# Kernel tuning notes

Measured on AMD Instinct MI355X. Metric: run time of the kernel, lower is better.

The kernel has to match this reference:

```python
import jax, jax.numpy as jnp
import numpy as np

QLEN, BSZ, DM, NH, DH, FF = 1024, 4, 512, 8, 64, 2048
EPS = 1e-5


def layer_norm(x, g, b):
    mu = x.mean(-1, keepdims=True)
    var = ((x - mu) ** 2).mean(-1, keepdims=True)
    return (x - mu) / jnp.sqrt(var + EPS) * g + b


def rel_pos_emb(qlen, klen, d_model, bsz):
    # XLNet-style 'bi' relative positional encoding: positions klen .. -qlen+1
    freq = jnp.arange(0, d_model, 2, dtype=jnp.float32)
    inv_freq = 1.0 / (10000.0 ** (freq / d_model))
    pos_seq = jnp.arange(klen, -qlen, -1, dtype=jnp.float32)  # [klen+qlen]
    sinusoid = pos_seq[:, None] * inv_freq[None, :]           # [klen+qlen, d/2]
    pe = jnp.concatenate([jnp.sin(sinusoid), jnp.cos(sinusoid)], -1)
    return jnp.broadcast_to(pe[:, None, :], (pe.shape[0], bsz, d_model))


def rel_shift(x, klen):
    # x: [q, p, b, n] with p = klen + qlen
    q, p, b, n = x.shape
    x = x.reshape(p, q, b, n)[1:]
    x = x.reshape(q, p - 1, b, n)[:, :klen]
    return x


def setup_inputs() -> dict:
    key = jax.random.key(0)
    ks = jax.random.split(key, 20)
    s = 0.02
    inp = {
        'src': jax.random.normal(ks[0], (QLEN, BSZ, DM), jnp.float32),
        'q_w': jax.random.normal(ks[1], (DM, NH, DH), jnp.float32) * s,
        'k_w': jax.random.normal(ks[2], (DM, NH, DH), jnp.float32) * s,
        'v_w': jax.random.normal(ks[3], (DM, NH, DH), jnp.float32) * s,
        'r_w': jax.random.normal(ks[4], (DM, NH, DH), jnp.float32) * s,
        'o_w': jax.random.normal(ks[5], (DM, NH, DH), jnp.float32) * s,
        'r_w_bias': jax.random.normal(ks[6], (NH, DH), jnp.float32) * s,
        'r_r_bias': jax.random.normal(ks[7], (NH, DH), jnp.float32) * s,
        'w1': jax.random.normal(ks[8], (FF, DM), jnp.float32) * s,
        'b1': jnp.zeros((FF,), jnp.float32),
        'w2': jax.random.normal(ks[9], (DM, FF), jnp.float32) * s,
        'b2': jnp.zeros((DM,), jnp.float32),
        'g1': jnp.ones((DM,), jnp.float32), 'be1': jnp.zeros((DM,), jnp.float32),
        'g2': jnp.ones((DM,), jnp.float32), 'be2': jnp.zeros((DM,), jnp.float32),
        'gf': jnp.ones((DM,), jnp.float32), 'bf': jnp.zeros((DM,), jnp.float32),
        'src_mask': jnp.triu(jnp.ones((QLEN, QLEN), bool), k=1),
    }
    return inp


def reference(src, q_w, k_w, v_w, r_w, o_w, r_w_bias, r_r_bias,
              w1, b1, w2, b2, g1, be1, g2, be2, gf, bf, src_mask):
    qlen, bsz, dm = src.shape
    klen = qlen  # mems=None
    scale = 1.0 / (DH ** 0.5)
    pos_emb = rel_pos_emb(qlen, klen, dm, bsz)  # [klen+qlen, b, d]
    mask = src_mask.astype(src.dtype)

    # --- RelativeMultiheadAttention (single weight-shared encoder layer) ---
    cat = src  # no memory
    q_head = jnp.einsum('ibh,hnd->ibnd', src, q_w)
    k_head = jnp.einsum('ibh,hnd->ibnd', cat, k_w)
    v_head = jnp.einsum('ibh,hnd->ibnd', cat, v_w)
    k_pos = jnp.einsum('ibh,hnd->ibnd', pos_emb, r_w)

    ac = jnp.einsum('ibnd,jbnd->ijbn', q_head + r_w_bias, k_head)
    bd = jnp.einsum('ibnd,jbnd->ijbn', q_head + r_r_bias, k_pos)
    bd = rel_shift(bd, klen)

    score = (ac + bd) * scale - 1e30 * mask[:, :, None, None]
    prob = jax.nn.softmax(score, axis=1)
    attn_vec = jnp.einsum('ijbn,jbnd->ibnd', prob, v_head)
    attn_out = jnp.einsum('ibnd,hnd->ibh', attn_vec, o_w)

    x = layer_norm(src + attn_out, g1, be1)
    ffn = jax.nn.gelu(x @ w1.T + b1, approximate=False) @ w2.T + b2
    x = layer_norm(x + ffn, g2, be2)

    # final encoder norm
    out = layer_norm(x, gf, bf)
    return out
```

## Files before the change

### kernel.cpp

```cpp
#include <hip/hip_runtime.h>

#define QLEN 1024
#define BSZ  4
#define DM   512
#define NH   8
#define DH   64
#define FFD  2048

static constexpr float LN_EPS = 1e-5f;

typedef __attribute__((ext_vector_type(8))) short short8_t;
typedef __attribute__((ext_vector_type(4))) float f32x4;

__device__ __forceinline__ ushort f2b(float f) {
  uint u = __float_as_uint(f);
  return (ushort)((u + 0x7FFFu + ((u >> 16) & 1u)) >> 16);
}
__device__ __forceinline__ float b2f(ushort h) {
  return __uint_as_float(((uint)h) << 16);
}

__global__ void pe_kernel(ushort* __restrict__ pe) {
  int idx = blockIdx.x * 256 + threadIdx.x;
  if (idx >= QLEN * DM) return;
  int r  = idx >> 9;
  int f  = idx & (DM - 1);
  int f0 = f & 255;
  float invf = __expf(-(float)f0 * (9.210340371976184f / 256.0f));
  float arg  = (float)r * invf;
  pe[idx] = f2b((f < 256) ? __sinf(arg) : __cosf(arg));
}

__global__ void cvt8_kernel(const float* __restrict__ in, ushort* __restrict__ out, int n8) {
  int idx = blockIdx.x * 256 + threadIdx.x;
  if (idx >= n8) return;
  const float4 f0 = *reinterpret_cast<const float4*>(in + (size_t)idx * 8);
  const float4 f1 = *reinterpret_cast<const float4*>(in + (size_t)idx * 8 + 4);
  uint p0 = f2b(f0.x) | ((uint)f2b(f0.y) << 16);
  uint p1 = f2b(f0.z) | ((uint)f2b(f0.w) << 16);
  uint p2 = f2b(f1.x) | ((uint)f2b(f1.y) << 16);
  uint p3 = f2b(f1.z) | ((uint)f2b(f1.w) << 16);
  int4 st; st.x = (int)p0; st.y = (int)p1; st.z = (int)p2; st.w = (int)p3;
  *reinterpret_cast<int4*>(out + (size_t)idx * 8) = st;
}

__global__ __launch_bounds__(256) void trans512_kernel(
    const float* __restrict__ qw, const float* __restrict__ kw,
    const float* __restrict__ vw, const float* __restrict__ rw,
    ushort* __restrict__ qkvw, ushort* __restrict__ rwT) {
  __shared__ float tile[32][33];
  const int z = blockIdx.z;
  const float* in = (z == 0) ? qw : (z == 1) ? kw : (z == 2) ? vw : rw;
  const int nd0 = blockIdx.x * 32, h0 = blockIdx.y * 32;
  const int tx = threadIdx.x & 31, ty = threadIdx.x >> 5;
#pragma unroll
  for (int k = 0; k < 4; ++k)
    tile[ty + 8 * k][tx] = in[(size_t)(h0 + ty + 8 * k) * 512 + nd0 + tx];
  __syncthreads();
  ushort* out = (z < 3) ? (qkvw + (size_t)z * 512 * 512) : rwT;
#pragma unroll
  for (int k = 0; k < 4; ++k)
    out[(size_t)(nd0 + ty + 8 * k) * 512 + h0 + tx] = f2b(tile[tx][ty + 8 * k]);
}

template <int EPI>
__global__ __launch_bounds__(256) void gemm_bf16(
    const ushort* __restrict__ A, const ushort* __restrict__ B,
    const float* __restrict__ bias, void* __restrict__ Cout,
    int M, int N, int K) {
  __shared__ ushort As[64 * 40];
  __shared__ ushort Bs[128 * 40];
  const int t = threadIdx.x;
  const int w = t >> 6, l = t & 63;
  const int lc = l & 15, lq = l >> 4;
  const int bm = blockIdx.y * 64, bn = blockIdx.x * 128;
  const int wr = (w >> 1) * 32, wc = (w & 1) * 64;
  const int sr = t >> 2, sk = (t & 3) * 8;

  f32x4 acc[2][4];
#pragma unroll
  for (int i = 0; i < 2; ++i)
#pragma unroll
    for (int j = 0; j < 4; ++j) acc[i][j] = (f32x4){0.f, 0.f, 0.f, 0.f};

  int4 a_v = *reinterpret_cast<const int4*>(A + (size_t)(bm + sr) * K + sk);
  int4 b0v = *reinterpret_cast<const int4*>(B + (size_t)(bn + sr) * K + sk);
  int4 b1v = *reinterpret_cast<const int4*>(B + (size_t)(bn + 64 + sr) * K + sk);

  for (int k0 = 0; k0 < K; k0 += 32) {
    *reinterpret_cast<int4*>(As + sr * 40 + sk) = a_v;
    *reinterpret_cast<int4*>(Bs + sr * 40 + sk) = b0v;
    *reinterpret_cast<int4*>(Bs + (64 + sr) * 40 + sk) = b1v;
    __syncthreads();
    if (k0 + 32 < K) {
      a_v = *reinterpret_cast<const int4*>(A + (size_t)(bm + sr) * K + k0 + 32 + sk);
      b0v = *reinterpret_cast<const int4*>(B + (size_t)(bn + sr) * K + k0 + 32 + sk);
      b1v = *reinterpret_cast<const int4*>(B + (size_t)(bn + 64 + sr) * K + k0 + 32 + sk);
    }
    short8_t af[2], bf[4];
#pragma unroll
    for (int mf = 0; mf < 2; ++mf)
      af[mf] = *reinterpret_cast<const short8_t*>(As + (wr + mf * 16 + lc) * 40 + lq * 8);
#pragma unroll
    for (int nf = 0; nf < 4; ++nf)
      bf[nf] = *reinterpret_cast<const short8_t*>(Bs + (wc + nf * 16 + lc) * 40 + lq * 8);
#pragma unroll
    for (int mf = 0; mf < 2; ++mf)
#pragma unroll
      for (int nf = 0; nf < 4; ++nf)
        acc[mf][nf] = __builtin_amdgcn_mfma_f32_16x16x32_bf16(af[mf], bf[nf], acc[mf][nf], 0, 0, 0);
    __syncthreads();
  }

#pragma unroll
  for (int mf = 0; mf < 2; ++mf)
#pragma unroll
    for (int nf = 0; nf < 4; ++nf) {
      const int col = bn + wc + nf * 16 + lc;
#pragma unroll
      for (int reg = 0; reg < 4; ++reg) {
        const int row = bm + wr + mf * 16 + lq * 4 + reg;
        float v = acc[mf][nf][reg];
        if (EPI == 2 || EPI == 3) v += bias[col];
        if (EPI == 2) v = 0.5f * v * (1.0f + erff(v * 0.70710678118654752f));
        if (EPI == 0 || EPI == 2)
          ((ushort*)Cout)[(size_t)row * N + col] = f2b(v);
        else
          ((float*)Cout)[(size_t)row * N + col] = v;
      }
    }
}

template <int EPI>
__global__ __launch_bounds__(256) void gemm128(
    const ushort* __restrict__ A, const ushort* __restrict__ B,
    const float* __restrict__ bias, void* __restrict__ Cout,
    int M, int N, int K) {
  __shared__ ushort As[128 * 40];
  __shared__ ushort Bs[128 * 40];
  const int t = threadIdx.x;
  const int w = t >> 6, l = t & 63;
  const int lc = l & 15, lq = l >> 4;
  const int bm = blockIdx.y * 128, bn = blockIdx.x * 128;
  const int wr = (w >> 1) * 64, wc = (w & 1) * 64;
  const int sr = t >> 2, sk = (t & 3) * 8;

  f32x4 acc[4][4];
#pragma unroll
  for (int i = 0; i < 4; ++i)
#pragma unroll
    for (int j = 0; j < 4; ++j) acc[i][j] = (f32x4){0.f, 0.f, 0.f, 0.f};

  int4 a0v = *reinterpret_cast<const int4*>(A + (size_t)(bm + sr) * K + sk);
  int4 a1v = *reinterpret_cast<const int4*>(A + (size_t)(bm + 64 + sr) * K + sk);
  int4 b0v = *reinterpret_cast<const int4*>(B + (size_t)(bn + sr) * K + sk);
  int4 b1v = *reinterpret_cast<const int4*>(B + (size_t)(bn + 64 + sr) * K + sk);

  for (int k0 = 0; k0 < K; k0 += 32) {
    *reinterpret_cast<int4*>(As + sr * 40 + sk) = a0v;
    *reinterpret_cast<int4*>(As + (64 + sr) * 40 + sk) = a1v;
    *reinterpret_cast<int4*>(Bs + sr * 40 + sk) = b0v;
    *reinterpret_cast<int4*>(Bs + (64 + sr) * 40 + sk) = b1v;
    __syncthreads();
    if (k0 + 32 < K) {
      a0v = *reinterpret_cast<const int4*>(A + (size_t)(bm + sr) * K + k0 + 32 + sk);
      a1v = *reinterpret_cast<const int4*>(A + (size_t)(bm + 64 + sr) * K + k0 + 32 + sk);
      b0v = *reinterpret_cast<const int4*>(B + (size_t)(bn + sr) * K + k0 + 32 + sk);
      b1v = *reinterpret_cast<const int4*>(B + (size_t)(bn + 64 + sr) * K + k0 + 32 + sk);
    }
    short8_t af[4], bf[4];
#pragma unroll
    for (int mf = 0; mf < 4; ++mf)
      af[mf] = *reinterpret_cast<const short8_t*>(As + (wr + mf * 16 + lc) * 40 + lq * 8);
#pragma unroll
    for (int nf = 0; nf < 4; ++nf)
      bf[nf] = *reinterpret_cast<const short8_t*>(Bs + (wc + nf * 16 + lc) * 40 + lq * 8);
#pragma unroll
    for (int mf = 0; mf < 4; ++mf)
#pragma unroll
      for (int nf = 0; nf < 4; ++nf)
        acc[mf][nf] = __builtin_amdgcn_mfma_f32_16x16x32_bf16(af[mf], bf[nf], acc[mf][nf], 0, 0, 0);
    __syncthreads();
  }

#pragma unroll
  for (int mf = 0; mf < 4; ++mf)
#pragma unroll
    for (int nf = 0; nf < 4; ++nf) {
      const int col = bn + wc + nf * 16 + lc;
#pragma unroll
      for (int reg = 0; reg < 4; ++reg) {
        const int row = bm + wr + mf * 16 + lq * 4 + reg;
        float v = acc[mf][nf][reg];
        if (EPI == 2 || EPI == 3) v += bias[col];
        if (EPI == 2) v = 0.5f * v * (1.0f + erff(v * 0.70710678118654752f));
        if (EPI == 0 || EPI == 2)
          ((ushort*)Cout)[(size_t)row * N + col] = f2b(v);
        else
          ((float*)Cout)[(size_t)row * N + col] = v;
      }
    }
}

__global__ __launch_bounds__(256) void gemm_split(
    const ushort* __restrict__ A, const ushort* __restrict__ B,
    float* __restrict__ Cout, int M, int N, int K, int halfK) {
  __shared__ ushort As[64 * 40];
  __shared__ ushort Bs[128 * 40];
  const int t = threadIdx.x;
  const int w = t >> 6, l = t & 63;
  const int lc = l & 15, lq = l >> 4;
  const int bm = blockIdx.y * 64, bn = blockIdx.x * 128;
  const int wr = (w >> 1) * 32, wc = (w & 1) * 64;
  const int sr = t >> 2, sk = (t & 3) * 8;
  const int kbeg = blockIdx.z * halfK, kend = kbeg + halfK;
  float* C = Cout + (size_t)blockIdx.z * M * N;

  f32x4 acc[2][4];
#pragma unroll
  for (int i = 0; i < 2; ++i)
#pragma unroll
    for (int j = 0; j < 4; ++j) acc[i][j] = (f32x4){0.f, 0.f, 0.f, 0.f};

  int4 a_v = *reinterpret_cast<const int4*>(A + (size_t)(bm + sr) * K + kbeg + sk);
  int4 b0v = *reinterpret_cast<const int4*>(B + (size_t)(bn + sr) * K + kbeg + sk);
  int4 b1v = *reinterpret_cast<const int4*>(B + (size_t)(bn + 64 + sr) * K + kbeg + sk);

  for (int k0 = kbeg; k0 < kend; k0 += 32) {
    *reinterpret_cast<int4*>(As + sr * 40 + sk) = a_v;
    *reinterpret_cast<int4*>(Bs + sr * 40 + sk) = b0v;
    *reinterpret_cast<int4*>(Bs + (64 + sr) * 40 + sk) = b1v;
    __syncthreads();
    if (k0 + 32 < kend) {
      a_v = *reinterpret_cast<const int4*>(A + (size_t)(bm + sr) * K + k0 + 32 + sk);
      b0v = *reinterpret_cast<const int4*>(B + (size_t)(bn + sr) * K + k0 + 32 + sk);
      b1v = *reinterpret_cast<const int4*>(B + (size_t)(bn + 64 + sr) * K + k0 + 32 + sk);
    }
    short8_t af[2], bf[4];
#pragma unroll
    for (int mf = 0; mf < 2; ++mf)
      af[mf] = *reinterpret_cast<const short8_t*>(As + (wr + mf * 16 + lc) * 40 + lq * 8);
#pragma unroll
    for (int nf = 0; nf < 4; ++nf)
      bf[nf] = *reinterpret_cast<const short8_t*>(Bs + (wc + nf * 16 + lc) * 40 + lq * 8);
#pragma unroll
    for (int mf = 0; mf < 2; ++mf)
#pragma unroll
      for (int nf = 0; nf < 4; ++nf)
        acc[mf][nf] = __builtin_amdgcn_mfma_f32_16x16x32_bf16(af[mf], bf[nf], acc[mf][nf], 0, 0, 0);
    __syncthreads();
  }

#pragma unroll
  for (int mf = 0; mf < 2; ++mf)
#pragma unroll
    for (int nf = 0; nf < 4; ++nf) {
      const int col = bn + wc + nf * 16 + lc;
#pragma unroll
      for (int reg = 0; reg < 4; ++reg) {
        const int row = bm + wr + mf * 16 + lq * 4 + reg;
        C[(size_t)row * N + col] = acc[mf][nf][reg];
      }
    }
}

__global__ __launch_bounds__(256) void repack_kernel(
    const ushort* __restrict__ qkv, const float* __restrict__ rwb,
    const float* __restrict__ rrb, ushort* __restrict__ qaF,
    ushort* __restrict__ qbF, ushort* __restrict__ kF, ushort* __restrict__ vF) {
  __shared__ ushort st[32][72];
  const int t = threadIdx.x, l = t & 63, lc = l & 15, lq = l >> 4;
  const int tile = blockIdx.x, head = blockIdx.y, role = blockIdx.z;
  const int b = head >> 3, n = head & 7;
  const int s0 = tile * 32;
  const int sec = (role == 0) ? 0 : (role == 1) ? 512 : 1024;
  {
    const int s = t >> 3, d8 = (t & 7) * 8;
    int4 rd = *reinterpret_cast<const int4*>(
        qkv + (size_t)((s0 + s) * 4 + b) * 1536 + sec + n * 64 + d8);
    *reinterpret_cast<int4*>(&st[s][d8]) = rd;
  }
  __syncthreads();
  if (role == 0) {
    const int f = t >> 6, sub = f >> 1, kc = f & 1;
    const int row = sub * 16 + lc, k = kc * 32 + lq * 8;
    short8_t qv = *reinterpret_cast<const short8_t*>(&st[row][k]);
    const float4 w0 = *reinterpret_cast<const float4*>(rwb + n * 64 + k);
    const float4 w1 = *reinterpret_cast<const float4*>(rwb + n * 64 + k + 4);
    const float4 u0 = *reinterpret_cast<const float4*>(rrb + n * 64 + k);
    const float4 u1 = *reinterpret_cast<const float4*>(rrb + n * 64 + k + 4);
    const float wv[8] = {w0.x, w0.y, w0.z, w0.w, w1.x, w1.y, w1.z, w1.w};
    const float uv[8] = {u0.x, u0.y, u0.z, u0.w, u1.x, u1.y, u1.z, u1.w};
    short8_t a_, b_;
#pragma unroll
    for (int e = 0; e < 8; ++e) {
      float q = b2f((ushort)qv[e]);
      a_[e] = (short)f2b(q + wv[e]);
      b_[e] = (short)f2b(q + uv[e]);
    }
    const size_t o = ((size_t)((head * 64 + tile * 2 + sub) * 2 + kc)) * 512 + l * 8;
    *reinterpret_cast<short8_t*>(qaF + o) = a_;
    *reinterpret_cast<short8_t*>(qbF + o) = b_;
  } else if (role == 1) {
    const int f = t >> 6, sub = f >> 1, kc = f & 1;
    const int row = sub * 16 + lc, k = kc * 32 + lq * 8;
    short8_t kv = *reinterpret_cast<const short8_t*>(&st[row][k]);
    const size_t o = ((size_t)((head * 64 + tile * 2 + sub) * 2 + kc)) * 512 + l * 8;
    *reinterpret_cast<short8_t*>(kF + o) = kv;
  } else {
    const int nf = t >> 6;
    short8_t vv;
#pragma unroll
    for (int e = 0; e < 8; ++e) vv[e] = (short)st[lq * 8 + e][nf * 16 + lc];
    const size_t o = ((size_t)((head * 32 + tile) * 4 + nf)) * 512 + l * 8;
    *reinterpret_cast<short8_t*>(vF + o) = vv;
  }
}

__global__ __launch_bounds__(128) void kprelF_kernel(
    const ushort* __restrict__ kprel, ushort* __restrict__ kprelF) {
  const int t = threadIdx.x, l = t & 63, lc = l & 15, lq = l >> 4;
  const int kc = t >> 6;
  const int m = blockIdx.x, n = blockIdx.y;
  const int rho = m * 16 - 31 + lc;
  short8_t v;
  if (rho >= 0 && rho < 1024)
    v = *reinterpret_cast<const short8_t*>(kprel + (size_t)rho * 512 + n * 64 + kc * 32 + lq * 8);
  else
#pragma unroll
    for (int e = 0; e < 8; ++e) v[e] = 0;
  const size_t o = ((size_t)((n * 66 + m) * 2 + kc)) * 512 + l * 8;
  *reinterpret_cast<short8_t*>(kprelF + o) = v;
}

__global__ __launch_bounds__(256, 4) void attn_mfma(
    const ushort* __restrict__ qaF, const ushort* __restrict__ qbF,
    const ushort* __restrict__ kF, const ushort* __restrict__ kpF,
    const ushort* __restrict__ vF, ushort* __restrict__ av) {
  __shared__ __align__(16) char smemU[22016];

  const int t = threadIdx.x, w = t >> 6, l = t & 63;
  const int lid = blockIdx.y * 32 + blockIdx.x;
  const int head = (lid & 7) * 4 + ((lid >> 3) & 3);
  const int pr   = lid >> 5;
  const int b = head >> 3, n = head & 7;
  const int lc = l & 15, lq = l >> 4;

  float*  gw = reinterpret_cast<float*>(smemU) + w * (16 * 66);
  ushort* pw = reinterpret_cast<ushort*>(smemU + 16896) + w * (16 * 40);

  for (int ph = 0; ph < 2; ++ph) {
    const int it = ph ? 63 - pr : pr;
    const int i0 = it * 16;
    __syncthreads();

    short8_t qa[2], qb[2];
    {
      const size_t qo = ((size_t)(head * 64 + it) * 2) * 512 + l * 8;
      qa[0] = *reinterpret_cast<const short8_t*>(qaF + qo);
      qa[1] = *reinterpret_cast<const short8_t*>(qaF + qo + 512);
      qb[0] = *reinterpret_cast<const short8_t*>(qbF + qo);
      qb[1] = *reinterpret_cast<const short8_t*>(qbF + qo + 512);
    }

    float m_run[4], l_run[4];
    f32x4 oacc[4];
#pragma unroll
    for (int reg = 0; reg < 4; ++reg) { m_run[reg] = -1e30f; l_run[reg] = 0.f; }
#pragma unroll
    for (int nf = 0; nf < 4; ++nf) oacc[nf] = (f32x4){0.f, 0.f, 0.f, 0.f};

    const int nj = it / 2 + 1;

    for (int jt = w; jt < nj; jt += 4) {
      const int j0 = jt * 32;
      const int D = i0 - j0;

      f32x4 sacc[2];
#pragma unroll
      for (int nf = 0; nf < 2; ++nf) sacc[nf] = (f32x4){0.f, 0.f, 0.f, 0.f};
#pragma unroll
      for (int kc = 0; kc < 2; ++kc)
#pragma unroll
        for (int nf = 0; nf < 2; ++nf) {
          short8_t kf = *reinterpret_cast<const short8_t*>(
              kF + ((size_t)((head * 64 + (j0 >> 4) + nf) * 2 + kc)) * 512 + l * 8);
          sacc[nf] = __builtin_amdgcn_mfma_f32_16x16x32_bf16(qa[kc], kf, sacc[nf], 0, 0, 0);
        }

      f32x4 gacc[3];
#pragma unroll
      for (int nf = 0; nf < 3; ++nf) gacc[nf] = (f32x4){0.f, 0.f, 0.f, 0.f};
#pragma unroll
      for (int kc = 0; kc < 2; ++kc)
#pragma unroll
        for (int nf = 0; nf < 3; ++nf) {
          short8_t pf = *reinterpret_cast<const short8_t*>(
              kpF + ((size_t)((n * 66 + (D >> 4) + nf) * 2 + kc)) * 512 + l * 8);
          gacc[nf] = __builtin_amdgcn_mfma_f32_16x16x32_bf16(qb[kc], pf, gacc[nf], 0, 0, 0);
        }

#pragma unroll
      for (int nf = 0; nf < 3; ++nf)
#pragma unroll
        for (int reg = 0; reg < 4; ++reg)
          gw[(lq * 4 + reg) * 66 + nf * 16 + lc] = gacc[nf][reg];

      float s0v[4], s1v[4];
#pragma unroll
      for (int reg = 0; reg < 4; ++reg) {
        const int r = lq * 4 + reg;
        const int c0 = lc, c1 = 16 + lc;
        float s0 = (sacc[0][reg] + gw[r * 66 + (r - c0 + 31)]) * 0.125f;
        float s1 = (sacc[1][reg] + gw[r * 66 + (r - c1 + 31)]) * 0.125f;
        if (D < 32) {
          if (c0 > D + r) s0 = -1e30f;
          if (c1 > D + r) s1 = -1e30f;
        }
        s0v[reg] = s0; s1v[reg] = s1;
      }
      bool ok = true;
#pragma unroll
      for (int reg = 0; reg < 4; ++reg)
        ok &= (fmaxf(s0v[reg], s1v[reg]) <= m_run[reg] + 8.0f);
      if (__all(ok ? 1 : 0)) {
#pragma unroll
        for (int reg = 0; reg < 4; ++reg) {
          const int r = lq * 4 + reg;
          const float p0 = __expf(s0v[reg] - m_run[reg]);
          const float p1 = __expf(s1v[reg] - m_run[reg]);
          float ps = p0 + p1;
          ps += __shfl_xor(ps, 1);
          ps += __shfl_xor(ps, 2);
          ps += __shfl_xor(ps, 4);
          ps += __shfl_xor(ps, 8);
          l_run[reg] += ps;
          pw[r * 40 + lc] = f2b(p0);
          pw[r * 40 + 16 + lc] = f2b(p1);
        }
      } else {
#pragma unroll
        for (int reg = 0; reg < 4; ++reg) {
          const int r = lq * 4 + reg;
          float tm = fmaxf(s0v[reg], s1v[reg]);
          tm = fmaxf(tm, __shfl_xor(tm, 1));
          tm = fmaxf(tm, __shfl_xor(tm, 2));
          tm = fmaxf(tm, __shfl_xor(tm, 4));
          tm = fmaxf(tm, __shfl_xor(tm, 8));
          const float mn = fmaxf(m_run[reg], tm);
          const float corr = __expf(m_run[reg] - mn);
          const float p0 = __expf(s0v[reg] - mn), p1 = __expf(s1v[reg] - mn);
          float ps = p0 + p1;
          ps += __shfl_xor(ps, 1);
          ps += __shfl_xor(ps, 2);
          ps += __shfl_xor(ps, 4);
          ps += __shfl_xor(ps, 8);
          l_run[reg] = l_run[reg] * corr + ps;
          m_run[reg] = mn;
#pragma unroll
          for (int nf = 0; nf < 4; ++nf) oacc[nf][reg] *= corr;
          pw[r * 40 + lc] = f2b(p0);
          pw[r * 40 + 16 + lc] = f2b(p1);
        }
      }

      short8_t pa = *reinterpret_cast<const short8_t*>(pw + lc * 40 + lq * 8);
#pragma unroll
      for (int nf = 0; nf < 4; ++nf) {
        short8_t vf = *reinterpret_cast<const short8_t*>(
            vF + ((size_t)((head * 32 + jt) * 4 + nf)) * 512 + l * 8);
        oacc[nf] = __builtin_amdgcn_mfma_f32_16x16x32_bf16(pa, vf, oacc[nf], 0, 0, 0);
      }
    }

    __syncthreads();
    float* obuf = reinterpret_cast<float*>(smemU);
    float* mlb  = reinterpret_cast<float*>(smemU + 4352);

    if (lc == 0) {
#pragma unroll
      for (int reg = 0; reg < 4; ++reg) {
        const int r = lq * 4 + reg;
        mlb[(w * 16 + r) * 2 + 0] = m_run[reg];
        mlb[(w * 16 + r) * 2 + 1] = l_run[reg];
      }
    }
    for (int i = t; i < 16 * 68; i += 256) obuf[i] = 0.f;
    __syncthreads();

    float scl[4];
#pragma unroll
    for (int reg = 0; reg < 4; ++reg) {
      const int r = lq * 4 + reg;
      const float m0 = mlb[r * 2], m1 = mlb[(16 + r) * 2],
                  m2 = mlb[(32 + r) * 2], m3 = mlb[(48 + r) * 2];
      const float ms = fmaxf(fmaxf(m0, m1), fmaxf(m2, m3));
      scl[reg] = __expf(mlb[(w * 16 + r) * 2] - ms);
    }
#pragma unroll
    for (int ww = 0; ww < 4; ++ww) {
      if (w == ww) {
#pragma unroll
        for (int nf = 0; nf < 4; ++nf)
#pragma unroll
          for (int reg = 0; reg < 4; ++reg) {
            const int r = lq * 4 + reg;
            obuf[r * 68 + nf * 16 + lc] += scl[reg] * oacc[nf][reg];
          }
      }
      __syncthreads();
    }

    {
      const int r = t >> 4, d0 = (t & 15) * 4;
      const float m0 = mlb[r * 2], m1 = mlb[(16 + r) * 2],
                  m2 = mlb[(32 + r) * 2], m3 = mlb[(48 + r) * 2];
      const float ms = fmaxf(fmaxf(m0, m1), fmaxf(m2, m3));
      const float ls = mlb[r * 2 + 1] * __expf(m0 - ms) + mlb[(16 + r) * 2 + 1] * __expf(m1 - ms) +
                       mlb[(32 + r) * 2 + 1] * __expf(m2 - ms) + mlb[(48 + r) * 2 + 1] * __expf(m3 - ms);
      const float inv = 1.f / ls;
      uint pk0 = (uint)f2b(obuf[r * 68 + d0] * inv) | ((uint)f2b(obuf[r * 68 + d0 + 1] * inv) << 16);
      uint pk1 = (uint)f2b(obuf[r * 68 + d0 + 2] * inv) | ((uint)f2b(obuf[r * 68 + d0 + 3] * inv) << 16);
      int2 st2; st2.x = (int)pk0; st2.y = (int)pk1;
      const int tok = (i0 + r) * 4 + b;
      *reinterpret_cast<int2*>(av + (size_t)tok * 512 + n * 64 + d0) = st2;
    }
  }
}

__device__ __forceinline__ float blk_sum(float v, volatile float* sb) {
  v += __shfl_xor(v, 1);  v += __shfl_xor(v, 2);  v += __shfl_xor(v, 4);
  v += __shfl_xor(v, 8);  v += __shfl_xor(v, 16); v += __shfl_xor(v, 32);
  const int t = threadIdx.x;
  if ((t & 63) == 0) sb[t >> 6] = v;
  __syncthreads();
  v = sb[0] + sb[1] + sb[2] + sb[3];
  __syncthreads();
  return v;
}

__global__ __launch_bounds__(256) void ln_res_kernel(
    const float* __restrict__ aoa, const float* __restrict__ aob,
    const float* __restrict__ res,
    const float* __restrict__ g, const float* __restrict__ be,
    float* __restrict__ out, ushort* __restrict__ outb) {
  __shared__ float sb[4];
  const int row = blockIdx.x, t = threadIdx.x;
  const size_t base = (size_t)row * DM;
  const float x0 = aoa[base + t] + aob[base + t] + res[base + t];
  const float x1 = aoa[base + t + 256] + aob[base + t + 256] + res[base + t + 256];
  const float mu = blk_sum(x0 + x1, sb) * (1.f / DM);
  const float d0 = x0 - mu, d1 = x1 - mu;
  const float var = blk_sum(d0 * d0 + d1 * d1, sb) * (1.f / DM);
  const float inv = rsqrtf(var + LN_EPS);
  const float z0 = d0 * inv * g[t] + be[t];
  const float z1 = d1 * inv * g[t + 256] + be[t + 256];
  out[base + t] = z0;
  out[base + t + 256] = z1;
  outb[base + t] = f2b(z0);
  outb[base + t + 256] = f2b(z1);
}

__global__ __launch_bounds__(256) void ln_final_kernel(
    const float* __restrict__ ya, const float* __restrict__ yb,
    const float* __restrict__ b2, const float* __restrict__ xres,
    const float* __restrict__ g2, const float* __restrict__ be2,
    const float* __restrict__ gf, const float* __restrict__ bf,
    float* __restrict__ out) {
  __shared__ float sb[4];
  const int row = blockIdx.x, t = threadIdx.x;
  const size_t base = (size_t)row * DM;
  const float x0 = ya[base + t] + yb[base + t] + b2[t] + xres[base + t];
  const float x1 = ya[base + t + 256] + yb[base + t + 256] + b2[t + 256] + xres[base + t + 256];
  const float mu = blk_sum(x0 + x1, sb) * (1.f / DM);
  const float d0 = x0 - mu, d1 = x1 - mu;
  const float var = blk_sum(d0 * d0 + d1 * d1, sb) * (1.f / DM);
  const float inv = rsqrtf(var + LN_EPS);
  const float z0 = d0 * inv * g2[t] + be2[t];
  const float z1 = d1 * inv * g2[t + 256] + be2[t + 256];
  const float mu2 = blk_sum(z0 + z1, sb) * (1.f / DM);
  const float e0 = z0 - mu2, e1 = z1 - mu2;
  const float var2 = blk_sum(e0 * e0 + e1 * e1, sb) * (1.f / DM);
  const float inv2 = rsqrtf(var2 + LN_EPS);
  out[base + t]       = e0 * inv2 * gf[t] + bf[t];
  out[base + t + 256] = e1 * inv2 * gf[t + 256] + bf[t + 256];
}

extern "C" void kernel_launch(void* const* d_in, const int* in_sizes, int n_in,
                              void* d_out, int out_size, void* d_ws, size_t ws_size,
                              hipStream_t stream) {
  const float* src = (const float*)d_in[0];
  const float* q_w = (const float*)d_in[1];
  const float* k_w = (const float*)d_in[2];
  const float* v_w = (const float*)d_in[3];
  const float* r_w = (const float*)d_in[4];
  const float* o_w = (const float*)d_in[5];
  const float* rwb = (const float*)d_in[6];
  const float* rrb = (const float*)d_in[7];
  const float* w1  = (const float*)d_in[8];
  const float* b1  = (const float*)d_in[9];
  const float* w2  = (const float*)d_in[10];
  const float* b2  = (const float*)d_in[11];
  const float* g1  = (const float*)d_in[12];
  const float* be1 = (const float*)d_in[13];
  const float* g2  = (const float*)d_in[14];
  const float* be2 = (const float*)d_in[15];
  const float* gf  = (const float*)d_in[16];
  const float* bf  = (const float*)d_in[17];

  char* ws = (char*)d_ws;
  const size_t KB = 1024, MB = 1024 * 1024;
  ushort* srcb   = (ushort*)(ws);
  ushort* qkvw   = (ushort*)(ws + 4 * MB);
  ushort* rwT    = (ushort*)(ws + 5 * MB + 512 * KB);
  ushort* owb    = (ushort*)(ws + 6 * MB);
  ushort* w1b    = (ushort*)(ws + 6 * MB + 512 * KB);
  ushort* w2b    = (ushort*)(ws + 8 * MB + 512 * KB);
  ushort* peb    = (ushort*)(ws + 10 * MB + 512 * KB);
  ushort* qkv    = (ushort*)(ws + 11 * MB + 512 * KB);
  ushort* kprel  = (ushort*)(ws + 23 * MB + 512 * KB);
  ushort* qaF    = (ushort*)(ws + 24 * MB + 512 * KB);
  ushort* qbF    = (ushort*)(ws + 28 * MB + 512 * KB);
  ushort* kF     = (ushort*)(ws + 32 * MB + 512 * KB);
  ushort* vF     = (ushort*)(ws + 36 * MB + 512 * KB);
  ushort* kprelF = (ushort*)(ws + 40 * MB + 512 * KB);
  ushort* av     = (ushort*)(ws + 42 * MB);
  float*  aoP    = (float*) (ws + 24 * MB + 512 * KB);
  float*  x1     = (float*) (ws + 46 * MB);
  ushort* x1b    = (ushort*)(ws + 42 * MB);
  ushort* h      = (ushort*)(ws + 11 * MB + 512 * KB);
  float*  y2P    = (float*) (ws + 27 * MB + 512 * KB);
  float*  outp   = (float*)d_out;

  pe_kernel<<<dim3(2048), 256, 0, stream>>>(peb);
  cvt8_kernel<<<dim3(1024), 256, 0, stream>>>(src, srcb, 262144);
  cvt8_kernel<<<dim3(128), 256, 0, stream>>>(o_w, owb, 32768);
  cvt8_kernel<<<dim3(512), 256, 0, stream>>>(w1, w1b, 131072);
  cvt8_kernel<<<dim3(512), 256, 0, stream>>>(w2, w2b, 131072);
  trans512_kernel<<<dim3(16, 16, 4), 256, 0, stream>>>(q_w, k_w, v_w, r_w, qkvw, rwT);

  gemm128<0><<<dim3(12, 32), 256, 0, stream>>>(srcb, qkvw, nullptr, qkv, 4096, 1536, 512);
  gemm_bf16<0><<<dim3(4, 16), 256, 0, stream>>>(peb, rwT, nullptr, kprel, 1024, 512, 512);

  repack_kernel<<<dim3(32, 32, 3), 256, 0, stream>>>(qkv, rwb, rrb, qaF, qbF, kF, vF);
  kprelF_kernel<<<dim3(66, 8), 128, 0, stream>>>(kprel, kprelF);

  attn_mfma<<<dim3(32, 32), 256, 0, stream>>>(qaF, qbF, kF, kprelF, vF, av);

  gemm_split<<<dim3(4, 64, 2), 256, 0, stream>>>(av, owb, aoP, 4096, 512, 512, 256);
  ln_res_kernel<<<dim3(4096), 256, 0, stream>>>(aoP, aoP + 2097152, src, g1, be1, x1, x1b);

  gemm128<2><<<dim3(16, 32), 256, 0, stream>>>(x1b, w1b, b1, h, 4096, 2048, 512);
  gemm_split<<<dim3(4, 64, 2), 256, 0, stream>>>(h, w2b, y2P, 4096, 512, 2048, 1024);

  ln_final_kernel<<<dim3(4096), 256, 0, stream>>>(y2P, y2P + 2097152, b2, x1, g2, be2, gf, bf, outp);
}
```

Measured before the change: 160.0 us.

## Widen attention key block to 64 and fuse prep kernels into one launch

The attention inner loop now processes 64 keys per wave iteration instead of 32. That halves the number of online-softmax rescale and reduction steps and gives more MFMA work per positional-band load. The positional K fragment layout is padded to 68 tiles with a 63 offset to match, and shared memory per block grows. Separately, the pe, cvt8 and transpose prep kernels are merged into one launch to cut launch overhead. The risks are coarser causal-tile granularity, which wastes masked work, and extra register and LDS pressure that could reduce occupancy.

```diff
diff --git a/kernel.cpp b/kernel.cpp
--- a/kernel.cpp
+++ b/kernel.cpp
@@ -20,20 +20,7 @@
   return __uint_as_float(((uint)h) << 16);
 }
 
-__global__ void pe_kernel(ushort* __restrict__ pe) {
-  int idx = blockIdx.x * 256 + threadIdx.x;
-  if (idx >= QLEN * DM) return;
-  int r  = idx >> 9;
-  int f  = idx & (DM - 1);
-  int f0 = f & 255;
-  float invf = __expf(-(float)f0 * (9.210340371976184f / 256.0f));
-  float arg  = (float)r * invf;
-  pe[idx] = f2b((f < 256) ? __sinf(arg) : __cosf(arg));
-}
-
-__global__ void cvt8_kernel(const float* __restrict__ in, ushort* __restrict__ out, int n8) {
-  int idx = blockIdx.x * 256 + threadIdx.x;
-  if (idx >= n8) return;
+__device__ __forceinline__ void cvt8_body(const float* in, ushort* out, int idx) {
   const float4 f0 = *reinterpret_cast<const float4*>(in + (size_t)idx * 8);
   const float4 f1 = *reinterpret_cast<const float4*>(in + (size_t)idx * 8 + 4);
   uint p0 = f2b(f0.x) | ((uint)f2b(f0.y) << 16);
@@ -44,23 +31,46 @@
   *reinterpret_cast<int4*>(out + (size_t)idx * 8) = st;
 }
 
-__global__ __launch_bounds__(256) void trans512_kernel(
+__global__ __launch_bounds__(256) void prep_kernel(
+    const float* __restrict__ src, const float* __restrict__ o_w,
+    const float* __restrict__ w1, const float* __restrict__ w2,
     const float* __restrict__ qw, const float* __restrict__ kw,
     const float* __restrict__ vw, const float* __restrict__ rw,
-    ushort* __restrict__ qkvw, ushort* __restrict__ rwT) {
+    ushort* __restrict__ peb, ushort* __restrict__ srcb,
+    ushort* __restrict__ owb, ushort* __restrict__ w1b,
+    ushort* __restrict__ w2b, ushort* __restrict__ qkvw,
+    ushort* __restrict__ rwT) {
   __shared__ float tile[32][33];
-  const int z = blockIdx.z;
-  const float* in = (z == 0) ? qw : (z == 1) ? kw : (z == 2) ? vw : rw;
-  const int nd0 = blockIdx.x * 32, h0 = blockIdx.y * 32;
-  const int tx = threadIdx.x & 31, ty = threadIdx.x >> 5;
-#pragma unroll
-  for (int k = 0; k < 4; ++k)
-    tile[ty + 8 * k][tx] = in[(size_t)(h0 + ty + 8 * k) * 512 + nd0 + tx];
-  __syncthreads();
-  ushort* out = (z < 3) ? (qkvw + (size_t)z * 512 * 512) : rwT;
-#pragma unroll
-  for (int k = 0; k < 4; ++k)
-    out[(size_t)(nd0 + ty + 8 * k) * 512 + h0 + tx] = f2b(tile[tx][ty + 8 * k]);
+  const int bid = blockIdx.x, t = threadIdx.x;
+  if (bid < 2048) {
+    const int idx = bid * 256 + t;
+    const int r = idx >> 9, f = idx & 511, f0 = f & 255;
+    float invf = __expf(-(float)f0 * (9.210340371976184f / 256.0f));
+    float arg  = (float)r * invf;
+    peb[idx] = f2b((f < 256) ? __sinf(arg) : __cosf(arg));
+  } else if (bid < 3072) {
+    cvt8_body(src, srcb, (bid - 2048) * 256 + t);
+  } else if (bid < 3200) {
+    cvt8_body(o_w, owb, (bid - 3072) * 256 + t);
+  } else if (bid < 3712) {
+    cvt8_body(w1, w1b, (bid - 3200) * 256 + t);
+  } else if (bid < 4224) {
+    cvt8_body(w2, w2b, (bid - 3712) * 256 + t);
+  } else {
+    const int e = bid - 4224;
+    const int z = e >> 8, rem = e & 255, bx = rem & 15, by = rem >> 4;
+    const float* in = (z == 0) ? qw : (z == 1) ? kw : (z == 2) ? vw : rw;
+    const int nd0 = bx * 32, h0 = by * 32;
+    const int tx = t & 31, ty = t >> 5;
+#pragma unroll
+    for (int k = 0; k < 4; ++k)
+      tile[ty + 8 * k][tx] = in[(size_t)(h0 + ty + 8 * k) * 512 + nd0 + tx];
+    __syncthreads();
+    ushort* out = (z < 3) ? (qkvw + (size_t)z * 512 * 512) : rwT;
+#pragma unroll
+    for (int k = 0; k < 4; ++k)
+      out[(size_t)(nd0 + ty + 8 * k) * 512 + h0 + tx] = f2b(tile[tx][ty + 8 * k]);
+  }
 }
 
 template <int EPI>
@@ -322,14 +332,14 @@
   const int t = threadIdx.x, l = t & 63, lc = l & 15, lq = l >> 4;
   const int kc = t >> 6;
   const int m = blockIdx.x, n = blockIdx.y;
-  const int rho = m * 16 - 31 + lc;
+  const int rho = m * 16 - 63 + lc;
   short8_t v;
   if (rho >= 0 && rho < 1024)
     v = *reinterpret_cast<const short8_t*>(kprel + (size_t)rho * 512 + n * 64 + kc * 32 + lq * 8);
   else
 #pragma unroll
     for (int e = 0; e < 8; ++e) v[e] = 0;
-  const size_t o = ((size_t)((n * 66 + m) * 2 + kc)) * 512 + l * 8;
+  const size_t o = ((size_t)((n * 68 + m) * 2 + kc)) * 512 + l * 8;
   *reinterpret_cast<short8_t*>(kprelF + o) = v;
 }
 
@@ -337,7 +347,7 @@
     const ushort* __restrict__ qaF, const ushort* __restrict__ qbF,
     const ushort* __restrict__ kF, const ushort* __restrict__ kpF,
     const ushort* __restrict__ vF, ushort* __restrict__ av) {
-  __shared__ __align__(16) char smemU[22016];
+  __shared__ __align__(16) char smemU[30720];
 
   const int t = threadIdx.x, w = t >> 6, l = t & 63;
   const int lid = blockIdx.y * 32 + blockIdx.x;
@@ -346,8 +356,8 @@
   const int b = head >> 3, n = head & 7;
   const int lc = l & 15, lq = l >> 4;
 
-  float*  gw = reinterpret_cast<float*>(smemU) + w * (16 * 66);
-  ushort* pw = reinterpret_cast<ushort*>(smemU + 16896) + w * (16 * 40);
+  float*  gw = reinterpret_cast<float*>(smemU + w * 5376);
+  ushort* pw = reinterpret_cast<ushort*>(smemU + 21504 + w * 2304);
 
   for (int ph = 0; ph < 2; ++ph) {
     const int it = ph ? 63 - pr : pr;
@@ -370,87 +380,91 @@
 #pragma unroll
     for (int nf = 0; nf < 4; ++nf) oacc[nf] = (f32x4){0.f, 0.f, 0.f, 0.f};
 
-    const int nj = it / 2 + 1;
-
-    for (int jt = w; jt < nj; jt += 4) {
-      const int j0 = jt * 32;
+    const int njb = (it >> 2) + 1;
+
+    for (int jb = w; jb < njb; jb += 4) {
+      const int j0 = jb * 64;
       const int D = i0 - j0;
 
-      f32x4 sacc[2];
-#pragma unroll
-      for (int nf = 0; nf < 2; ++nf) sacc[nf] = (f32x4){0.f, 0.f, 0.f, 0.f};
+      f32x4 sacc[4];
+#pragma unroll
+      for (int nf = 0; nf < 4; ++nf) sacc[nf] = (f32x4){0.f, 0.f, 0.f, 0.f};
 #pragma unroll
       for (int kc = 0; kc < 2; ++kc)
 #pragma unroll
-        for (int nf = 0; nf < 2; ++nf) {
+        for (int nf = 0; nf < 4; ++nf) {
           short8_t kf = *reinterpret_cast<const short8_t*>(
               kF + ((size_t)((head * 64 + (j0 >> 4) + nf) * 2 + kc)) * 512 + l * 8);
           sacc[nf] = __builtin_amdgcn_mfma_f32_16x16x32_bf16(qa[kc], kf, sacc[nf], 0, 0, 0);
         }
 
-      f32x4 gacc[3];
-#pragma unroll
-      for (int nf = 0; nf < 3; ++nf) gacc[nf] = (f32x4){0.f, 0.f, 0.f, 0.f};
+      f32x4 gacc[5];
+#pragma unroll
+      for (int nf = 0; nf < 5; ++nf) gacc[nf] = (f32x4){0.f, 0.f, 0.f, 0.f};
 #pragma unroll
       for (int kc = 0; kc < 2; ++kc)
 #pragma unroll
-        for (int nf = 0; nf < 3; ++nf) {
+        for (int nf = 0; nf < 5; ++nf) {
           short8_t pf = *reinterpret_cast<const short8_t*>(
-              kpF + ((size_t)((n * 66 + (D >> 4) + nf) * 2 + kc)) * 512 + l * 8);
+              kpF + ((size_t)((n * 68 + (D >> 4) + nf) * 2 + kc)) * 512 + l * 8);
           gacc[nf] = __builtin_amdgcn_mfma_f32_16x16x32_bf16(qb[kc], pf, gacc[nf], 0, 0, 0);
         }
 
 #pragma unroll
-      for (int nf = 0; nf < 3; ++nf)
+      for (int nf = 0; nf < 5; ++nf)
 #pragma unroll
         for (int reg = 0; reg < 4; ++reg)
-          gw[(lq * 4 + reg) * 66 + nf * 16 + lc] = gacc[nf][reg];
-
-      float s0v[4], s1v[4];
-#pragma unroll
-      for (int reg = 0; reg < 4; ++reg) {
-        const int r = lq * 4 + reg;
-        const int c0 = lc, c1 = 16 + lc;
-        float s0 = (sacc[0][reg] + gw[r * 66 + (r - c0 + 31)]) * 0.125f;
-        float s1 = (sacc[1][reg] + gw[r * 66 + (r - c1 + 31)]) * 0.125f;
-        if (D < 32) {
-          if (c0 > D + r) s0 = -1e30f;
-          if (c1 > D + r) s1 = -1e30f;
-        }
-        s0v[reg] = s0; s1v[reg] = s1;
-      }
-      bool ok = true;
-#pragma unroll
-      for (int reg = 0; reg < 4; ++reg)
-        ok &= (fmaxf(s0v[reg], s1v[reg]) <= m_run[reg] + 8.0f);
-      if (__all(ok ? 1 : 0)) {
+          gw[(lq * 4 + reg) * 84 + nf * 16 + lc] = gacc[nf][reg];
+
+      float sv[4][4];
+#pragma unroll
+      for (int nf = 0; nf < 4; ++nf)
 #pragma unroll
         for (int reg = 0; reg < 4; ++reg) {
           const int r = lq * 4 + reg;
-          const float p0 = __expf(s0v[reg] - m_run[reg]);
-          const float p1 = __expf(s1v[reg] - m_run[reg]);
-          float ps = p0 + p1;
+          const int c = nf * 16 + lc;
+          float s = (sacc[nf][reg] + gw[r * 84 + (r - c + 63)]) * 0.125f;
+          if (D < 64 && c > D + r) s = -1e30f;
+          sv[nf][reg] = s;
+        }
+
+      float rowmax[4];
+#pragma unroll
+      for (int reg = 0; reg < 4; ++reg)
+        rowmax[reg] = fmaxf(fmaxf(sv[0][reg], sv[1][reg]), fmaxf(sv[2][reg], sv[3][reg]));
+      bool ok = true;
+#pragma unroll
+      for (int reg = 0; reg < 4; ++reg) ok &= (rowmax[reg] <= m_run[reg] + 8.0f);
+
+      if (__all(ok ? 1 : 0)) {
+#pragma unroll
+        for (int reg = 0; reg < 4; ++reg) {
+          const int r = lq * 4 + reg;
+          float p[4], ps = 0.f;
+#pragma unroll
+          for (int nf = 0; nf < 4; ++nf) { p[nf] = __expf(sv[nf][reg] - m_run[reg]); ps += p[nf]; }
           ps += __shfl_xor(ps, 1);
           ps += __shfl_xor(ps, 2);
           ps += __shfl_xor(ps, 4);
           ps += __shfl_xor(ps, 8);
           l_run[reg] += ps;
-          pw[r * 40 + lc] = f2b(p0);
-          pw[r * 40 + 16 + lc] = f2b(p1);
+#pragma unroll
+          for (int nf = 0; nf < 4; ++nf) pw[r * 72 + nf * 16 + lc] = f2b(p[nf]);
         }
       } else {
 #pragma unroll
         for (int reg = 0; reg < 4; ++reg) {
           const int r = lq * 4 + reg;
-          float tm = fmaxf(s0v[reg], s1v[reg]);
+          float tm = rowmax[reg];
           tm = fmaxf(tm, __shfl_xor(tm, 1));
           tm = fmaxf(tm, __shfl_xor(tm, 2));
           tm = fmaxf(tm, __shfl_xor(tm, 4));
           tm = fmaxf(tm, __shfl_xor(tm, 8));
           const float mn = fmaxf(m_run[reg], tm);
           const float corr = __expf(m_run[reg] - mn);
-          const float p0 = __expf(s0v[reg] - mn), p1 = __expf(s1v[reg] - mn);
-          float ps = p0 + p1;
+          float p[4], ps = 0.f;
+#pragma unroll
+          for (int nf = 0; nf < 4; ++nf) { p[nf] = __expf(sv[nf][reg] - mn); ps += p[nf]; }
           ps += __shfl_xor(ps, 1);
           ps += __shfl_xor(ps, 2);
           ps += __shfl_xor(ps, 4);
@@ -459,18 +473,22 @@
           m_run[reg] = mn;
 #pragma unroll
           for (int nf = 0; nf < 4; ++nf) oacc[nf][reg] *= corr;
-          pw[r * 40 + lc] = f2b(p0);
-          pw[r * 40 + 16 + lc] = f2b(p1);
+#pragma unroll
+          for (int nf = 0; nf < 4; ++nf) pw[r * 72 + nf * 16 + lc] = f2b(p[nf]);
         }
       }
 
-      short8_t pa = *reinterpret_cast<const short8_t*>(pw + lc * 40 + lq * 8);
-#pragma unroll
-      for (int nf = 0; nf < 4; ++nf) {
-        short8_t vf = *reinterpret_cast<const short8_t*>(
-            vF + ((size_t)((head * 32 + jt) * 4 + nf)) * 512 + l * 8);
-        oacc[nf] = __builtin_amdgcn_mfma_f32_16x16x32_bf16(pa, vf, oacc[nf], 0, 0, 0);
-      }
+      short8_t pa[2];
+      pa[0] = *reinterpret_cast<const short8_t*>(pw + lc * 72 + lq * 8);
+      pa[1] = *reinterpret_cast<const short8_t*>(pw + lc * 72 + 32 + lq * 8);
+#pragma unroll
+      for (int ks = 0; ks < 2; ++ks)
+#pragma unroll
+        for (int nf = 0; nf < 4; ++nf) {
+          short8_t vf = *reinterpret_cast<const short8_t*>(
+              vF + ((size_t)((head * 32 + jb * 2 + ks) * 4 + nf)) * 512 + l * 8);
+          oacc[nf] = __builtin_amdgcn_mfma_f32_16x16x32_bf16(pa[ks], vf, oacc[nf], 0, 0, 0);
+        }
     }
 
     __syncthreads();
@@ -632,18 +650,14 @@
   float*  y2P    = (float*) (ws + 27 * MB + 512 * KB);
   float*  outp   = (float*)d_out;
 
-  pe_kernel<<<dim3(2048), 256, 0, stream>>>(peb);
-  cvt8_kernel<<<dim3(1024), 256, 0, stream>>>(src, srcb, 262144);
-  cvt8_kernel<<<dim3(128), 256, 0, stream>>>(o_w, owb, 32768);
-  cvt8_kernel<<<dim3(512), 256, 0, stream>>>(w1, w1b, 131072);
-  cvt8_kernel<<<dim3(512), 256, 0, stream>>>(w2, w2b, 131072);
-  trans512_kernel<<<dim3(16, 16, 4), 256, 0, stream>>>(q_w, k_w, v_w, r_w, qkvw, rwT);
+  prep_kernel<<<dim3(5248), 256, 0, stream>>>(src, o_w, w1, w2, q_w, k_w, v_w, r_w,
+                                              peb, srcb, owb, w1b, w2b, qkvw, rwT);
 
   gemm128<0><<<dim3(12, 32), 256, 0, stream>>>(srcb, qkvw, nullptr, qkv, 4096, 1536, 512);
   gemm_bf16<0><<<dim3(4, 16), 256, 0, stream>>>(peb, rwT, nullptr, kprel, 1024, 512, 512);
 
   repack_kernel<<<dim3(32, 32, 3), 256, 0, stream>>>(qkv, rwb, rrb, qaF, qbF, kF, vF);
-  kprelF_kernel<<<dim3(66, 8), 128, 0, stream>>>(kprel, kprelF);
+  kprelF_kernel<<<dim3(68, 8), 128, 0, stream>>>(kprel, kprelF);
 
   attn_mfma<<<dim3(32, 32), 256, 0, stream>>>(qaF, qbF, kF, kprelF, vF, av);
 
```

Result: slower. 169.9 us (+6.2%).
